# Performance work log

Hardware: AMD Instinct MI355X
Metric: run time of the kernel (lower is better)

The kernel has to match this reference:

```python
import jax, jax.numpy as jnp
import numpy as np
import math

D, NH, NL, NP_ = 256, 8, 3, 4
BS, LQ = 32, 300
SHAPES = [(80, 80), (40, 40), (20, 20)]
LV = sum(h * w for h, w in SHAPES)  # 8400
DFF = 1024


def _offset_bias():
    # faithful to MSDeformableAttention._reset_parameters
    thetas = jnp.arange(NH, dtype=jnp.float32) * (2.0 * math.pi / NH)
    grid = jnp.stack([jnp.cos(thetas), jnp.sin(thetas)], -1)
    grid = grid / jnp.abs(grid).max(-1, keepdims=True)
    grid = jnp.tile(grid.reshape(NH, 1, 1, 2), (1, NL, NP_, 1))
    grid = grid * jnp.arange(1, NP_ + 1, dtype=jnp.float32).reshape(1, 1, -1, 1)
    return grid.reshape(-1)


def setup_inputs() -> dict:
    key = jax.random.key(0)
    ks = iter(jax.random.split(key, 64))
    rn = lambda shape, s=0.02: jax.random.normal(next(ks), shape, jnp.float32) * s
    z = lambda n: jnp.zeros((n,), jnp.float32)
    o = lambda n: jnp.ones((n,), jnp.float32)
    inp = {
        'tgt': jax.random.normal(next(ks), (BS, LQ, D), jnp.float32),
        'reference_points': jax.random.uniform(next(ks), (BS, LQ, NL, 2), jnp.float32),
        'memory': jax.random.normal(next(ks), (BS, LV, D), jnp.float32),
        'query_pos_embed': jax.random.normal(next(ks), (BS, LQ, D), jnp.float32),
        'memory_spatial_shapes': np.array(SHAPES, dtype=np.int64),
        'memory_level_start_index': np.array([0, 6400, 8000], dtype=np.int64),
        # self-attn
        'Wq': rn((D, D)), 'bq': z(D), 'Wk': rn((D, D)), 'bk': z(D),
        'Wv': rn((D, D)), 'bv': z(D), 'Wo': rn((D, D)), 'bo': z(D),
        'ln1_g': o(D), 'ln1_b': z(D),
        # deformable cross-attn
        'W_vproj': rn((D, D)), 'b_vproj': z(D),
        'W_off': rn((D, NH * NL * NP_ * 2), 0.001), 'b_off': _offset_bias(),
        'W_attn': rn((D, NH * NL * NP_)), 'b_attn': z(NH * NL * NP_),
        'W_out': rn((D, D)), 'b_out': z(D),
        'ln2_g': o(D), 'ln2_b': z(D),
        # FFN
        'W1': rn((D, DFF)), 'b1': z(DFF), 'W2': rn((DFF, D)), 'b2': z(D),
        'ln3_g': o(D), 'ln3_b': z(D),
    }
    return inp


def _ln(x, g, b):
    m = x.mean(-1, keepdims=True)
    v = ((x - m) ** 2).mean(-1, keepdims=True)
    return (x - m) / jnp.sqrt(v + 1e-5) * g + b


def _ms_deform(value, shapes, loc, aw):
    # value [bs,Lv,nh,c]; loc [bs,Lq,nh,NL,NP,2] in [0,1]; aw [bs,Lq,nh,NL,NP]
    bs, Lv, nh, c = value.shape
    Lq = loc.shape[1]
    npts = loc.shape[4]
    grids = 2.0 * loc - 1.0
    out = jnp.zeros((bs, nh, Lq, c), value.dtype)
    start = 0
    for lvl, (h, w) in enumerate(shapes):
        flat = value[:, start:start + h * w].transpose(0, 2, 1, 3)  # [bs,nh,hw,c]
        start += h * w
        g = grids[:, :, :, lvl].transpose(0, 2, 1, 3, 4).reshape(bs, nh, Lq * npts, 2)
        # align_corners=False pixel coords
        x = (g[..., 0] + 1.0) * (w / 2.0) - 0.5
        y = (g[..., 1] + 1.0) * (h / 2.0) - 0.5
        x0 = jnp.floor(x); y0 = jnp.floor(y)
        wx1 = x - x0; wy1 = y - y0
        samp = jnp.zeros((bs, nh, Lq * npts, c), value.dtype)
        for xi, yi, wgt in ((x0, y0, (1 - wx1) * (1 - wy1)),
                            (x0 + 1, y0, wx1 * (1 - wy1)),
                            (x0, y0 + 1, (1 - wx1) * wy1),
                            (x0 + 1, y0 + 1, wx1 * wy1)):
            valid = (xi >= 0) & (xi < w) & (yi >= 0) & (yi < h)
            idx = (jnp.clip(yi, 0, h - 1) * w + jnp.clip(xi, 0, w - 1)).astype(jnp.int32)
            idx = jnp.broadcast_to(idx[..., None], idx.shape + (c,))
            gv = jnp.take_along_axis(flat, idx, axis=2)  # [bs,nh,Lq*np,c]
            samp = samp + gv * (wgt * valid.astype(value.dtype))[..., None]
        samp = samp.reshape(bs, nh, Lq, npts, c)
        a = aw[:, :, :, lvl].transpose(0, 2, 1, 3)  # [bs,nh,Lq,np]
        out = out + (samp * a[..., None]).sum(3)
    return out.transpose(0, 2, 1, 3).reshape(bs, Lq, nh * c)


def reference(tgt, reference_points, memory, query_pos_embed,
              memory_spatial_shapes, memory_level_start_index,
              Wq, bq, Wk, bk, Wv, bv, Wo, bo, ln1_g, ln1_b,
              W_vproj, b_vproj, W_off, b_off, W_attn, b_attn, W_out, b_out,
              ln2_g, ln2_b, W1, b1, W2, b2, ln3_g, ln3_b):
    shapes = [(int(h), int(w)) for h, w in np.asarray(memory_spatial_shapes)]
    bs, Lq, d = tgt.shape
    hd = d // NH
    # --- self attention (dropout=eval identity, attn_mask=None) ---
    q = tgt + query_pos_embed
    qh = (q @ Wq + bq).reshape(bs, Lq, NH, hd)
    kh = (q @ Wk + bk).reshape(bs, Lq, NH, hd)
    vh = (tgt @ Wv + bv).reshape(bs, Lq, NH, hd)
    att = jax.nn.softmax(jnp.einsum('bqhd,bkhd->bhqk', qh, kh) / jnp.sqrt(jnp.float32(hd)), axis=-1)
    sa = jnp.einsum('bhqk,bkhd->bqhd', att, vh).reshape(bs, Lq, d) @ Wo + bo
    tgt = _ln(tgt + sa, ln1_g, ln1_b)
    # --- deformable cross attention ---
    qc = tgt + query_pos_embed
    value = (memory @ W_vproj + b_vproj).reshape(bs, -1, NH, hd)
    off = (qc @ W_off + b_off).reshape(bs, Lq, NH, NL, NP_, 2)
    aw = jax.nn.softmax((qc @ W_attn + b_attn).reshape(bs, Lq, NH, NL * NP_), axis=-1)
    aw = aw.reshape(bs, Lq, NH, NL, NP_)
    norm = jnp.array([[w, h] for h, w in shapes], jnp.float32)  # flip -> (w,h)
    loc = reference_points[:, :, None, :, None, :] + off / norm[None, None, None, :, None, :]
    ca = _ms_deform(value, shapes, loc, aw) @ W_out + b_out
    tgt = _ln(tgt + ca, ln2_g, ln2_b)
    # --- FFN ---
    h = jax.nn.relu(tgt @ W1 + b1) @ W2 + b2
    return _ln(tgt + h, ln3_g, ln3_b)
```

## Files before the change

kernel.cpp:

```cpp
#include <hip/hip_runtime.h>
#include <hip/hip_bf16.h>

#define D_      256
#define NH_     8
#define HD_     32
#define NL_     3
#define NP_4    4
#define BS_     32
#define LQ_     300
#define LV_     8400
#define DFF_    1024
#define NTOK    (BS_ * LQ_)
#define NVAL    (BS_ * LV_)

typedef __attribute__((ext_vector_type(8))) short bf16x8;
typedef __attribute__((ext_vector_type(4))) float f32x4;

__device__ inline unsigned short f2bf(float x) {
    union { float f; unsigned u; } v; v.f = x;
    unsigned r = v.u + 0x7FFFu + ((v.u >> 16) & 1u);
    return (unsigned short)(r >> 16);
}
__device__ inline float bf2f(unsigned short x) {
    union { unsigned u; float f; } v; v.u = ((unsigned)x) << 16;
    return v.f;
}

struct TrDesc { const float* W; unsigned short* Wt; int K; int N; };
struct TrPack { TrDesc d[10]; };

__global__ __launch_bounds__(256)
void tr_kernel(TrPack p) {
    TrDesc d = p.d[blockIdx.z];
    const int n0 = blockIdx.x * 32, k0 = blockIdx.y * 32;
    if (n0 >= d.N || k0 >= d.K) return;
    __shared__ float t[32][33];
    const int tx = threadIdx.x & 31, ty = threadIdx.x >> 5;
    #pragma unroll
    for (int i = 0; i < 4; ++i) {
        int k = k0 + ty + i * 8, n = n0 + tx;
        t[ty + i * 8][tx] = (k < d.K && n < d.N) ? d.W[(size_t)k * d.N + n] : 0.f;
    }
    __syncthreads();
    #pragma unroll
    for (int i = 0; i < 4; ++i) {
        int n = n0 + ty + i * 8, k = k0 + tx;
        if (n < d.N && k < d.K) d.Wt[(size_t)n * d.K + k] = f2bf(t[tx][ty + i * 8]);
    }
}

template <int ROWS, int COLS, int KK, int KC, int WR, int WC, int AMODE, int CMODE>
__global__ __launch_bounds__(256, 4)
void gemm_os(const void* __restrict__ Ain,
             const unsigned short* __restrict__ Wt, const float* __restrict__ bias,
             void* __restrict__ Cout, int M, int N) {
    constexpr int LDK = KC + 8;
    constexpr int NC = KK / KC;
    constexpr int KS = KC / 32;
    constexpr int WROWS = ROWS / WR, WCOLS = COLS / WC;
    constexpr int RT = WROWS / 16, TC = WCOLS / 16;
    __shared__ unsigned short Alds[ROWS * LDK];
    __shared__ unsigned short Blds[COLS * LDK];

    const int tid = threadIdx.x, lane = tid & 63, w = tid >> 6;
    const int quad = lane >> 4, l16 = lane & 15;
    const int wr = w / WC, wc = w % WC;
    const int rowBase = blockIdx.y * ROWS;
    const int colBase = blockIdx.x * COLS;

    f32x4 acc[RT][TC];
    #pragma unroll
    for (int rt = 0; rt < RT; ++rt)
        #pragma unroll
        for (int j = 0; j < TC; ++j)
            #pragma unroll
            for (int r = 0; r < 4; ++r) acc[rt][j][r] = 0.f;

    for (int ch = 0; ch < NC; ++ch) {
        if (NC > 1) __syncthreads();
        if (AMODE == 2) {
            constexpr int CNT2 = ROWS * KC / 2048;
            #pragma unroll
            for (int i = 0; i < CNT2; ++i) {
                int idx = i * 256 + tid;
                int row = idx / (KC / 8), kofs = (idx % (KC / 8)) * 8;
                int4 v = *(const int4*)((const unsigned short*)Ain +
                          (size_t)(rowBase + row) * KK + ch * KC + kofs);
                *(int4*)&Alds[row * LDK + kofs] = v;
            }
        } else {
            constexpr int CNT = ROWS * KC / 1024;
            #pragma unroll
            for (int i = 0; i < CNT; ++i) {
                int idx = i * 256 + tid;
                int row = idx / (KC / 4), kofs = (idx % (KC / 4)) * 4;
                size_t gg = (size_t)(rowBase + row) * KK + ch * KC + kofs;
                float4 a = *(const float4*)((const float*)Ain + gg);
                ushort4 s4;
                s4.x = f2bf(a.x); s4.y = f2bf(a.y);
                s4.z = f2bf(a.z); s4.w = f2bf(a.w);
                *(ushort4*)&Alds[row * LDK + kofs] = s4;
            }
        }
        {
            constexpr int CNT = COLS * KC / 2048;
            #pragma unroll
            for (int i = 0; i < CNT; ++i) {
                int idx = i * 256 + tid;
                int col = idx / (KC / 8), kofs = (idx % (KC / 8)) * 8;
                int4 v = *(const int4*)(Wt + (size_t)(colBase + col) * KK + ch * KC + kofs);
                *(int4*)&Blds[col * LDK + kofs] = v;
            }
        }
        __syncthreads();

        #pragma unroll
        for (int s = 0; s < KS; ++s) {
            bf16x8 af[RT], bfr[TC];
            #pragma unroll
            for (int rt = 0; rt < RT; ++rt)
                af[rt] = *(const bf16x8*)&Alds[(wr * WROWS + rt * 16 + l16) * LDK + s * 32 + quad * 8];
            #pragma unroll
            for (int j = 0; j < TC; ++j)
                bfr[j] = *(const bf16x8*)&Blds[(wc * WCOLS + j * 16 + l16) * LDK + s * 32 + quad * 8];
            #pragma unroll
            for (int rt = 0; rt < RT; ++rt)
                #pragma unroll
                for (int j = 0; j < TC; ++j)
                    acc[rt][j] = __builtin_amdgcn_mfma_f32_16x16x32_bf16(af[rt], bfr[j], acc[rt][j], 0, 0, 0);
        }
    }

    #pragma unroll
    for (int rt = 0; rt < RT; ++rt) {
        #pragma unroll
        for (int j = 0; j < TC; ++j) {
            int col = colBase + wc * WCOLS + j * 16 + l16;
            float bb = bias[col];
            #pragma unroll
            for (int r = 0; r < 4; ++r) {
                int row = rowBase + wr * WROWS + rt * 16 + quad * 4 + r;
                float c = acc[rt][j][r] + bb;
                if (CMODE == 3) c = fmaxf(c, 0.f);
                if (CMODE >= 2)
                    ((unsigned short*)Cout)[(size_t)row * N + col] = f2bf(c);
                else
                    ((float*)Cout)[(size_t)row * N + col] = c;
            }
        }
    }
}

struct GDesc { const float* Ain; const float* A2; const unsigned short* Wt;
               const float* bias; void* Cout; int N; };
struct GPack3 { GDesc d[3]; };

template <int ROWS, int COLS, int KK, int KC, int WR, int WC, int CMODE>
__global__ __launch_bounds__(256, 4)
void gemm_osb(GPack3 pk) {
    constexpr int LDK = KC + 8;
    constexpr int NC = KK / KC;
    constexpr int KS = KC / 32;
    constexpr int WROWS = ROWS / WR, WCOLS = COLS / WC;
    constexpr int RT = WROWS / 16, TC = WCOLS / 16;
    __shared__ unsigned short Alds[ROWS * LDK];
    __shared__ unsigned short Blds[COLS * LDK];

    GDesc g = pk.d[blockIdx.z];
    const int colBase = blockIdx.x * COLS;
    if (colBase >= g.N) return;
    const int tid = threadIdx.x, lane = tid & 63, w = tid >> 6;
    const int quad = lane >> 4, l16 = lane & 15;
    const int wr = w / WC, wc = w % WC;
    const int rowBase = blockIdx.y * ROWS;

    f32x4 acc[RT][TC];
    #pragma unroll
    for (int rt = 0; rt < RT; ++rt)
        #pragma unroll
        for (int j = 0; j < TC; ++j)
            #pragma unroll
            for (int r = 0; r < 4; ++r) acc[rt][j][r] = 0.f;

    for (int ch = 0; ch < NC; ++ch) {
        if (NC > 1) __syncthreads();
        {
            constexpr int CNT = ROWS * KC / 1024;
            #pragma unroll
            for (int i = 0; i < CNT; ++i) {
                int idx = i * 256 + tid;
                int row = idx / (KC / 4), kofs = (idx % (KC / 4)) * 4;
                size_t gg = (size_t)(rowBase + row) * KK + ch * KC + kofs;
                float4 a = *(const float4*)(g.Ain + gg);
                if (g.A2) {
                    float4 b = *(const float4*)(g.A2 + gg);
                    a.x += b.x; a.y += b.y; a.z += b.z; a.w += b.w;
                }
                ushort4 s4;
                s4.x = f2bf(a.x); s4.y = f2bf(a.y);
                s4.z = f2bf(a.z); s4.w = f2bf(a.w);
                *(ushort4*)&Alds[row * LDK + kofs] = s4;
            }
        }
        {
            constexpr int CNT = COLS * KC / 2048;
            #pragma unroll
            for (int i = 0; i < CNT; ++i) {
                int idx = i * 256 + tid;
                int col = idx / (KC / 8), kofs = (idx % (KC / 8)) * 8;
                int4 v = *(const int4*)(g.Wt + (size_t)(colBase + col) * KK + ch * KC + kofs);
                *(int4*)&Blds[col * LDK + kofs] = v;
            }
        }
        __syncthreads();

        #pragma unroll
        for (int s = 0; s < KS; ++s) {
            bf16x8 af[RT], bfr[TC];
            #pragma unroll
            for (int rt = 0; rt < RT; ++rt)
                af[rt] = *(const bf16x8*)&Alds[(wr * WROWS + rt * 16 + l16) * LDK + s * 32 + quad * 8];
            #pragma unroll
            for (int j = 0; j < TC; ++j)
                bfr[j] = *(const bf16x8*)&Blds[(wc * WCOLS + j * 16 + l16) * LDK + s * 32 + quad * 8];
            #pragma unroll
            for (int rt = 0; rt < RT; ++rt)
                #pragma unroll
                for (int j = 0; j < TC; ++j)
                    acc[rt][j] = __builtin_amdgcn_mfma_f32_16x16x32_bf16(af[rt], bfr[j], acc[rt][j], 0, 0, 0);
        }
    }

    #pragma unroll
    for (int rt = 0; rt < RT; ++rt) {
        #pragma unroll
        for (int j = 0; j < TC; ++j) {
            int col = colBase + wc * WCOLS + j * 16 + l16;
            float bb = g.bias[col];
            #pragma unroll
            for (int r = 0; r < 4; ++r) {
                int row = rowBase + wr * WROWS + rt * 16 + quad * 4 + r;
                float c = acc[rt][j][r] + bb;
                if (CMODE >= 2)
                    ((unsigned short*)g.Cout)[(size_t)row * g.N + col] = f2bf(c);
                else
                    ((float*)g.Cout)[(size_t)row * g.N + col] = c;
            }
        }
    }
}

template <int KK, int KC>
__global__ __launch_bounds__(256)
void gemm_ln(const unsigned short* __restrict__ Ain,
             const unsigned short* __restrict__ Wt, const float* __restrict__ bias,
             const float* __restrict__ xres, const float* __restrict__ lng,
             const float* __restrict__ lnb, float* __restrict__ Cout) {
    constexpr int ROWS = 32, COLS = 256;
    constexpr int LDK = KC + 8;
    constexpr int NC = KK / KC;
    constexpr int KS = KC / 32;
    constexpr int RT = 2, TC = 4;
    __shared__ unsigned short Alds[ROWS * LDK];
    __shared__ unsigned short Blds[COLS * LDK];
    __shared__ float redS[4][32];
    __shared__ float redQ[4][32];

    const int tid = threadIdx.x, lane = tid & 63, w = tid >> 6;
    const int quad = lane >> 4, l16 = lane & 15;
    const int wc = w;
    const int rowBase = blockIdx.x * ROWS;

    f32x4 acc[RT][TC];
    #pragma unroll
    for (int rt = 0; rt < RT; ++rt)
        #pragma unroll
        for (int j = 0; j < TC; ++j)
            #pragma unroll
            for (int r = 0; r < 4; ++r) acc[rt][j][r] = 0.f;

    for (int ch = 0; ch < NC; ++ch) {
        if (NC > 1) __syncthreads();
        {
            constexpr int CNT2 = ROWS * KC / 2048;
            #pragma unroll
            for (int i = 0; i < CNT2; ++i) {
                int idx = i * 256 + tid;
                int row = idx / (KC / 8), kofs = (idx % (KC / 8)) * 8;
                int4 v = *(const int4*)(Ain + (size_t)(rowBase + row) * KK + ch * KC + kofs);
                *(int4*)&Alds[row * LDK + kofs] = v;
            }
        }
        {
            constexpr int CNT = COLS * KC / 2048;
            #pragma unroll
            for (int i = 0; i < CNT; ++i) {
                int idx = i * 256 + tid;
                int col = idx / (KC / 8), kofs = (idx % (KC / 8)) * 8;
                int4 v = *(const int4*)(Wt + (size_t)col * KK + ch * KC + kofs);
                *(int4*)&Blds[col * LDK + kofs] = v;
            }
        }
        __syncthreads();

        #pragma unroll
        for (int s = 0; s < KS; ++s) {
            bf16x8 af[RT], bfr[TC];
            #pragma unroll
            for (int rt = 0; rt < RT; ++rt)
                af[rt] = *(const bf16x8*)&Alds[(rt * 16 + l16) * LDK + s * 32 + quad * 8];
            #pragma unroll
            for (int j = 0; j < TC; ++j)
                bfr[j] = *(const bf16x8*)&Blds[(wc * 64 + j * 16 + l16) * LDK + s * 32 + quad * 8];
            #pragma unroll
            for (int rt = 0; rt < RT; ++rt)
                #pragma unroll
                for (int j = 0; j < TC; ++j)
                    acc[rt][j] = __builtin_amdgcn_mfma_f32_16x16x32_bf16(af[rt], bfr[j], acc[rt][j], 0, 0, 0);
        }
    }

    float p[RT][4], q[RT][4];
    #pragma unroll
    for (int rt = 0; rt < RT; ++rt)
        #pragma unroll
        for (int r = 0; r < 4; ++r) { p[rt][r] = 0.f; q[rt][r] = 0.f; }

    #pragma unroll
    for (int rt = 0; rt < RT; ++rt) {
        #pragma unroll
        for (int j = 0; j < TC; ++j) {
            int col = wc * 64 + j * 16 + l16;
            float bb = bias[col];
            #pragma unroll
            for (int r = 0; r < 4; ++r) {
                int row = rowBase + rt * 16 + quad * 4 + r;
                float v = acc[rt][j][r] + bb + xres[(size_t)row * 256 + col];
                acc[rt][j][r] = v;
                p[rt][r] += v;
                q[rt][r] += v * v;
            }
        }
    }
    #pragma unroll
    for (int rt = 0; rt < RT; ++rt)
        #pragma unroll
        for (int r = 0; r < 4; ++r)
            #pragma unroll
            for (int off = 1; off < 16; off <<= 1) {
                p[rt][r] += __shfl_xor(p[rt][r], off);
                q[rt][r] += __shfl_xor(q[rt][r], off);
            }
    if (l16 == 0) {
        #pragma unroll
        for (int rt = 0; rt < RT; ++rt)
            #pragma unroll
            for (int r = 0; r < 4; ++r) {
                redS[w][rt * 16 + quad * 4 + r] = p[rt][r];
                redQ[w][rt * 16 + quad * 4 + r] = q[rt][r];
            }
    }
    __syncthreads();
    #pragma unroll
    for (int rt = 0; rt < RT; ++rt) {
        #pragma unroll
        for (int r = 0; r < 4; ++r) {
            int ridx = rt * 16 + quad * 4 + r;
            float s  = redS[0][ridx] + redS[1][ridx] + redS[2][ridx] + redS[3][ridx];
            float ss = redQ[0][ridx] + redQ[1][ridx] + redQ[2][ridx] + redQ[3][ridx];
            float mean = s * (1.0f / 256.0f);
            float var  = ss * (1.0f / 256.0f) - mean * mean;
            float inv  = rsqrtf(var + 1e-5f);
            int row = rowBase + ridx;
            #pragma unroll
            for (int j = 0; j < TC; ++j) {
                int col = wc * 64 + j * 16 + l16;
                Cout[(size_t)row * 256 + col] =
                    (acc[rt][j][r] - mean) * inv * lng[col] + lnb[col];
            }
        }
    }
}

#define PS_STRIDE 344
__global__ __launch_bounds__(256)
void attn_mfma(const unsigned short* __restrict__ qh,
               const unsigned short* __restrict__ kh,
               const unsigned short* __restrict__ vh,
               unsigned short* __restrict__ out) {
    __shared__ unsigned short Ps[4 * 16 * PS_STRIDE];
    __shared__ unsigned short Vs[32 * PS_STRIDE];
    const int tid = threadIdx.x;
    const int bh = blockIdx.x >> 1, half_ = blockIdx.x & 1;
    const int b = bh >> 3, h = bh & 7;
    const int w = tid >> 6, lane = tid & 63;
    const int quad = lane >> 4, l16 = lane & 15;

    for (int i = tid; i < 4 * 16 * PS_STRIDE / 2; i += 256) ((unsigned*)Ps)[i] = 0u;

    const size_t hbase = ((size_t)b * LQ_) * D_ + h * HD_;
    for (int it = 0; it < 10; ++it) {
        int chunk = tid + 256 * it;
        int key = chunk >> 3, cc = (chunk & 7) * 4;
        ushort4 v = make_ushort4(0, 0, 0, 0);
        if (key < LQ_) v = *(const ushort4*)(vh + hbase + (size_t)key * D_ + cc);
        Vs[(cc + 0) * PS_STRIDE + key] = v.x;
        Vs[(cc + 1) * PS_STRIDE + key] = v.y;
        Vs[(cc + 2) * PS_STRIDE + key] = v.z;
        Vs[(cc + 3) * PS_STRIDE + key] = v.w;
    }
    __syncthreads();

    const unsigned short* qb = qh + hbase;
    const unsigned short* kb = kh + hbase;
    const float scale = 0.17677669529663687f;

    for (int qt = 10 * half_ + w; qt < 10 * half_ + 10 && qt < 19; qt += 4) {
        int rowq = qt * 16 + l16; if (rowq > LQ_ - 1) rowq = LQ_ - 1;
        bf16x8 aq = *(const bf16x8*)(qb + (size_t)rowq * D_ + quad * 8);

        f32x4 S[19];
        #pragma unroll
        for (int kt = 0; kt < 19; ++kt) {
            int rowk = kt * 16 + l16; if (rowk > LQ_ - 1) rowk = LQ_ - 1;
            bf16x8 bk = *(const bf16x8*)(kb + (size_t)rowk * D_ + quad * 8);
            f32x4 z; z[0] = z[1] = z[2] = z[3] = 0.f;
            S[kt] = __builtin_amdgcn_mfma_f32_16x16x32_bf16(aq, bk, z, 0, 0, 0);
        }
        float mrow[4] = {-1e30f, -1e30f, -1e30f, -1e30f};
        #pragma unroll
        for (int kt = 0; kt < 19; ++kt) {
            bool masked = (kt == 18) && (l16 >= 12);
            #pragma unroll
            for (int r = 0; r < 4; ++r) {
                float s = masked ? -1e30f : S[kt][r] * scale;
                S[kt][r] = s;
                mrow[r] = fmaxf(mrow[r], s);
            }
        }
        #pragma unroll
        for (int r = 0; r < 4; ++r)
            #pragma unroll
            for (int off = 1; off < 16; off <<= 1)
                mrow[r] = fmaxf(mrow[r], __shfl_xor(mrow[r], off));
        float psum[4] = {0.f, 0.f, 0.f, 0.f};
        #pragma unroll
        for (int kt = 0; kt < 19; ++kt)
            #pragma unroll
            for (int r = 0; r < 4; ++r) {
                float pcur = __expf(S[kt][r] - mrow[r]);
                S[kt][r] = pcur;
                psum[r] += pcur;
            }
        #pragma unroll
        for (int r = 0; r < 4; ++r)
            #pragma unroll
            for (int off = 1; off < 16; off <<= 1)
                psum[r] += __shfl_xor(psum[r], off);
        float linv[4];
        #pragma unroll
        for (int r = 0; r < 4; ++r) linv[r] = 1.f / psum[r];

        unsigned short* pw = Ps + w * (16 * PS_STRIDE);
        #pragma unroll
        for (int kt = 0; kt < 19; ++kt)
            #pragma unroll
            for (int r = 0; r < 4; ++r)
                pw[(quad * 4 + r) * PS_STRIDE + kt * 16 + l16] = f2bf(S[kt][r]);

        f32x4 o0, o1;
        #pragma unroll
        for (int r = 0; r < 4; ++r) { o0[r] = 0.f; o1[r] = 0.f; }
        #pragma unroll
        for (int ks = 0; ks < 10; ++ks) {
            bf16x8 ap = *(const bf16x8*)(pw + l16 * PS_STRIDE + ks * 32 + quad * 8);
            bf16x8 b0 = *(const bf16x8*)(Vs + l16 * PS_STRIDE + ks * 32 + quad * 8);
            bf16x8 b1 = *(const bf16x8*)(Vs + (16 + l16) * PS_STRIDE + ks * 32 + quad * 8);
            o0 = __builtin_amdgcn_mfma_f32_16x16x32_bf16(ap, b0, o0, 0, 0, 0);
            o1 = __builtin_amdgcn_mfma_f32_16x16x32_bf16(ap, b1, o1, 0, 0, 0);
        }
        #pragma unroll
        for (int r = 0; r < 4; ++r) {
            int q = qt * 16 + quad * 4 + r;
            if (q < LQ_) {
                size_t ob = ((size_t)b * LQ_ + q) * D_ + h * HD_;
                out[ob + l16]      = f2bf(o0[r] * linv[r]);
                out[ob + 16 + l16] = f2bf(o1[r] * linv[r]);
            }
        }
    }
}

__global__ __launch_bounds__(256)
void deform_kernel(const unsigned short* __restrict__ value,
                   const float* __restrict__ off,
                   const float* __restrict__ awl,
                   const float* __restrict__ ref,
                   unsigned short* __restrict__ out) {
    const int lvl_hw[3]    = {80, 40, 20};
    const int lvl_start[3] = {0, 6400, 8000};
    const int gid = blockIdx.x * 16 + (threadIdx.x >> 4);
    const int c2  = (threadIdx.x & 15) * 2;
    const int h   = gid & 7;
    const int bq  = gid >> 3;
    const int b   = bq / LQ_;

    float lg[12];
    const float* ap = awl + (size_t)bq * 96 + h * 12;
    float m = -1e30f;
    #pragma unroll
    for (int j = 0; j < 12; ++j) { lg[j] = ap[j]; m = fmaxf(m, lg[j]); }
    float s = 0.f;
    #pragma unroll
    for (int j = 0; j < 12; ++j) { lg[j] = __expf(lg[j] - m); s += lg[j]; }
    const float inv = 1.0f / s;

    const float* op = off + (size_t)bq * 192 + h * 24;
    const float* rp = ref + (size_t)bq * 6;

    float accx = 0.f, accy = 0.f;
    #pragma unroll
    for (int l = 0; l < NL_; ++l) {
        const int W = lvl_hw[l], H = lvl_hw[l];
        const float fw = (float)W, fh = (float)H;
        const float rx = rp[l * 2 + 0], ry = rp[l * 2 + 1];
        const unsigned short* vbase =
            value + ((size_t)b * LV_ + lvl_start[l]) * D_ + h * HD_ + c2;
        #pragma unroll
        for (int p = 0; p < NP_4; ++p) {
            float ox = op[(l * 4 + p) * 2 + 0], oy = op[(l * 4 + p) * 2 + 1];
            float x = (rx + ox / fw) * fw - 0.5f;
            float y = (ry + oy / fh) * fh - 0.5f;
            float x0f = floorf(x), y0f = floorf(y);
            float wx = x - x0f, wy = y - y0f;
            int x0 = (int)x0f, y0 = (int)y0f;
            float a = lg[l * 4 + p] * inv;
            const float cw[4] = {a * (1.f - wx) * (1.f - wy), a * wx * (1.f - wy),
                                 a * (1.f - wx) * wy,         a * wx * wy};
            const int cx[4] = {x0, x0 + 1, x0,     x0 + 1};
            const int cy[4] = {y0, y0,     y0 + 1, y0 + 1};
            #pragma unroll
            for (int cor = 0; cor < 4; ++cor) {
                int xi = cx[cor], yi = cy[cor];
                if (xi < 0 || xi >= W || yi < 0 || yi >= H) continue;
                unsigned v = *(const unsigned*)(vbase + (size_t)(yi * W + xi) * D_);
                accx += cw[cor] * bf2f((unsigned short)(v & 0xFFFFu));
                accy += cw[cor] * bf2f((unsigned short)(v >> 16));
            }
        }
    }
    unsigned pack = (unsigned)f2bf(accx) | ((unsigned)f2bf(accy) << 16);
    *(unsigned*)(out + (size_t)bq * D_ + h * HD_ + c2) = pack;
}

extern "C" void kernel_launch(void* const* d_in, const int* in_sizes, int n_in,
                              void* d_out, int out_size, void* d_ws, size_t ws_size,
                              hipStream_t stream) {
    const float* tgt   = (const float*)d_in[0];
    const float* refpt = (const float*)d_in[1];
    const float* mem   = (const float*)d_in[2];
    const float* qpos  = (const float*)d_in[3];
    const float* Wq = (const float*)d_in[6],  *bq = (const float*)d_in[7];
    const float* Wk = (const float*)d_in[8],  *bk = (const float*)d_in[9];
    const float* Wv = (const float*)d_in[10], *bv = (const float*)d_in[11];
    const float* Wo = (const float*)d_in[12], *bo = (const float*)d_in[13];
    const float* ln1_g = (const float*)d_in[14], *ln1_b = (const float*)d_in[15];
    const float* W_vproj = (const float*)d_in[16], *b_vproj = (const float*)d_in[17];
    const float* W_off  = (const float*)d_in[18], *b_off  = (const float*)d_in[19];
    const float* W_attn = (const float*)d_in[20], *b_attn = (const float*)d_in[21];
    const float* W_out  = (const float*)d_in[22], *b_out  = (const float*)d_in[23];
    const float* ln2_g = (const float*)d_in[24], *ln2_b = (const float*)d_in[25];
    const float* W1 = (const float*)d_in[26], *b1 = (const float*)d_in[27];
    const float* W2 = (const float*)d_in[28], *b2 = (const float*)d_in[29];
    const float* ln3_g = (const float*)d_in[30], *ln3_b = (const float*)d_in[31];
    float* out = (float*)d_out;

    char* p = (char*)d_ws;
    const size_t TOKD = (size_t)NTOK * D_;
    float* buf_attn = (float*)p; p += TOKD * 4;
    float* buf_tmp  = (float*)p; p += TOKD * 4;
    float* buf_t1   = (float*)p; p += TOKD * 4;
    float* buf_t2   = (float*)p; p += TOKD * 4;
    unsigned short* buf_qh = (unsigned short*)p; p += TOKD * 2;
    unsigned short* buf_kh = (unsigned short*)p; p += TOKD * 2;
    unsigned short* buf_vh = (unsigned short*)p; p += TOKD * 2;
    float* buf_off  = (float*)p; p += (size_t)NTOK * 192 * 4;
    float* buf_awl  = (float*)p; p += (size_t)NTOK * 96 * 4;
    unsigned short* wt_q   = (unsigned short*)p; p += 65536 * 2;
    unsigned short* wt_k   = (unsigned short*)p; p += 65536 * 2;
    unsigned short* wt_v   = (unsigned short*)p; p += 65536 * 2;
    unsigned short* wt_o   = (unsigned short*)p; p += 65536 * 2;
    unsigned short* wt_vp  = (unsigned short*)p; p += 65536 * 2;
    unsigned short* wt_off = (unsigned short*)p; p += 49152 * 2;
    unsigned short* wt_awl = (unsigned short*)p; p += 24576 * 2;
    unsigned short* wt_out = (unsigned short*)p; p += 65536 * 2;
    unsigned short* wt_1   = (unsigned short*)p; p += (size_t)262144 * 2;
    unsigned short* wt_2   = (unsigned short*)p; p += (size_t)262144 * 2;
    unsigned short* buf_value = (unsigned short*)p;
    unsigned short* buf_ffnb  = (unsigned short*)p;

    TrPack pk;
    pk.d[0] = {Wq,      wt_q,   256, 256};
    pk.d[1] = {Wk,      wt_k,   256, 256};
    pk.d[2] = {Wv,      wt_v,   256, 256};
    pk.d[3] = {Wo,      wt_o,   256, 256};
    pk.d[4] = {W_vproj, wt_vp,  256, 256};
    pk.d[5] = {W_off,   wt_off, 256, 192};
    pk.d[6] = {W_attn,  wt_awl, 256, 96};
    pk.d[7] = {W_out,   wt_out, 256, 256};
    pk.d[8] = {W1,      wt_1,   256, 1024};
    pk.d[9] = {W2,      wt_2,   1024, 256};
    tr_kernel<<<dim3(32, 32, 10), 256, 0, stream>>>(pk);

    GPack3 qkv;
    qkv.d[0] = {tgt, qpos,    wt_q, bq, buf_qh, 256};
    qkv.d[1] = {tgt, qpos,    wt_k, bk, buf_kh, 256};
    qkv.d[2] = {tgt, nullptr, wt_v, bv, buf_vh, 256};
    gemm_osb<32, 128, 256, 128, 1, 4, 2><<<dim3(2, NTOK / 32, 3), 256, 0, stream>>>(qkv);
    attn_mfma<<<BS_ * NH_ * 2, 256, 0, stream>>>(buf_qh, buf_kh, buf_vh,
                                                 (unsigned short*)buf_attn);
    gemm_ln<256, 128><<<NTOK / 32, 256, 0, stream>>>(
        (const unsigned short*)buf_attn, wt_o, bo, tgt, ln1_g, ln1_b, buf_t1);

    gemm_os<64, 128, 256, 128, 2, 2, 0, 2><<<dim3(2, NVAL / 64), 256, 0, stream>>>(
        mem, wt_vp, b_vproj, buf_value, NVAL, 256);
    GPack3 oa;
    oa.d[0] = {buf_t1, qpos, wt_off, b_off,  buf_off, 192};
    oa.d[1] = {buf_t1, qpos, wt_awl, b_attn, buf_awl, 96};
    oa.d[2] = oa.d[1];
    gemm_osb<32, 96, 256, 128, 2, 2, 0><<<dim3(2, NTOK / 32, 2), 256, 0, stream>>>(oa);
    deform_kernel<<<(BS_ * LQ_ * NH_) / 16, 256, 0, stream>>>(
        buf_value, buf_off, buf_awl, refpt, (unsigned short*)buf_attn);
    gemm_ln<256, 128><<<NTOK / 32, 256, 0, stream>>>(
        (const unsigned short*)buf_attn, wt_out, b_out, buf_t1, ln2_g, ln2_b, buf_t2);

    gemm_os<32, 128, 256, 128, 1, 4, 0, 3><<<dim3(8, NTOK / 32), 256, 0, stream>>>(
        buf_t2, wt_1, b1, buf_ffnb, NTOK, DFF_);
    gemm_ln<1024, 128><<<NTOK / 32, 256, 0, stream>>>(
        buf_ffnb, wt_2, b2, buf_t2, ln3_g, ln3_b, out);
}
```

Baseline: 680.6 us.

## Stream fp32 activations straight into MFMA registers, keep weights in LDS

Replaces the LDS-staged gemm_os and the QKV gemm_osb with a streaming GEMM. The full K=256 weight slice for 128 columns sits in LDS, while each wave loads its 32 rows of fp32 activations directly from global memory into registers. Those activations are converted to bf16 in registers and fed to MFMA, with a software pipeline that prefetches two K-chunks ahead. This drops A-tile LDS staging and the per-chunk barriers and uses larger 128-row blocks, in exchange for higher register pressure, a lower occupancy bound of 2, and uncoalesced strided global reads of A. NTOK=9600 divides evenly by 128, so the 128-row tiling stays valid for the token GEMMs.

```diff
diff --git a/kernel.cpp b/kernel.cpp
--- a/kernel.cpp
+++ b/kernel.cpp
@@ -49,97 +49,126 @@
     }
 }
 
-template <int ROWS, int COLS, int KK, int KC, int WR, int WC, int AMODE, int CMODE>
-__global__ __launch_bounds__(256, 4)
-void gemm_os(const void* __restrict__ Ain,
-             const unsigned short* __restrict__ Wt, const float* __restrict__ bias,
-             void* __restrict__ Cout, int M, int N) {
-    constexpr int LDK = KC + 8;
-    constexpr int NC = KK / KC;
-    constexpr int KS = KC / 32;
-    constexpr int WROWS = ROWS / WR, WCOLS = COLS / WC;
-    constexpr int RT = WROWS / 16, TC = WCOLS / 16;
-    __shared__ unsigned short Alds[ROWS * LDK];
-    __shared__ unsigned short Blds[COLS * LDK];
+template <int COLS, int AMODE, int CMODE>
+__device__ inline void gemm_stream_body(
+        const float* __restrict__ Ain, const float* __restrict__ A2,
+        const unsigned short* __restrict__ Wt, const float* __restrict__ bias,
+        void* __restrict__ Cout, int N, int colBase, int rowBase,
+        unsigned short* Blds) {
+    constexpr int LDK = 264;
+    constexpr int TC = COLS / 16;
 
     const int tid = threadIdx.x, lane = tid & 63, w = tid >> 6;
     const int quad = lane >> 4, l16 = lane & 15;
-    const int wr = w / WC, wc = w % WC;
-    const int rowBase = blockIdx.y * ROWS;
-    const int colBase = blockIdx.x * COLS;
-
-    f32x4 acc[RT][TC];
-    #pragma unroll
-    for (int rt = 0; rt < RT; ++rt)
+
+    {
+        constexpr int CNT = COLS / 8;
+        #pragma unroll
+        for (int i = 0; i < CNT; ++i) {
+            int idx = i * 256 + tid;
+            int col = idx >> 5, kofs = (idx & 31) * 8;
+            int4 v = *(const int4*)(Wt + (size_t)(colBase + col) * 256 + kofs);
+            *(int4*)&Blds[col * LDK + kofs] = v;
+        }
+    }
+    __syncthreads();
+
+    const int r0 = rowBase + w * 32 + l16;
+    const int r1 = r0 + 16;
+
+    f32x4 acc[2][TC];
+    #pragma unroll
+    for (int rt = 0; rt < 2; ++rt)
         #pragma unroll
         for (int j = 0; j < TC; ++j)
             #pragma unroll
             for (int r = 0; r < 4; ++r) acc[rt][j][r] = 0.f;
 
-    for (int ch = 0; ch < NC; ++ch) {
-        if (NC > 1) __syncthreads();
-        if (AMODE == 2) {
-            constexpr int CNT2 = ROWS * KC / 2048;
-            #pragma unroll
-            for (int i = 0; i < CNT2; ++i) {
-                int idx = i * 256 + tid;
-                int row = idx / (KC / 8), kofs = (idx % (KC / 8)) * 8;
-                int4 v = *(const int4*)((const unsigned short*)Ain +
-                          (size_t)(rowBase + row) * KK + ch * KC + kofs);
-                *(int4*)&Alds[row * LDK + kofs] = v;
-            }
-        } else {
-            constexpr int CNT = ROWS * KC / 1024;
-            #pragma unroll
-            for (int i = 0; i < CNT; ++i) {
-                int idx = i * 256 + tid;
-                int row = idx / (KC / 4), kofs = (idx % (KC / 4)) * 4;
-                size_t gg = (size_t)(rowBase + row) * KK + ch * KC + kofs;
-                float4 a = *(const float4*)((const float*)Ain + gg);
-                ushort4 s4;
-                s4.x = f2bf(a.x); s4.y = f2bf(a.y);
-                s4.z = f2bf(a.z); s4.w = f2bf(a.w);
-                *(ushort4*)&Alds[row * LDK + kofs] = s4;
-            }
-        }
-        {
-            constexpr int CNT = COLS * KC / 2048;
-            #pragma unroll
-            for (int i = 0; i < CNT; ++i) {
-                int idx = i * 256 + tid;
-                int col = idx / (KC / 8), kofs = (idx % (KC / 8)) * 8;
-                int4 v = *(const int4*)(Wt + (size_t)(colBase + col) * KK + ch * KC + kofs);
-                *(int4*)&Blds[col * LDK + kofs] = v;
-            }
-        }
-        __syncthreads();
-
-        #pragma unroll
-        for (int s = 0; s < KS; ++s) {
-            bf16x8 af[RT], bfr[TC];
-            #pragma unroll
-            for (int rt = 0; rt < RT; ++rt)
-                af[rt] = *(const bf16x8*)&Alds[(wr * WROWS + rt * 16 + l16) * LDK + s * 32 + quad * 8];
-            #pragma unroll
-            for (int j = 0; j < TC; ++j)
-                bfr[j] = *(const bf16x8*)&Blds[(wc * WCOLS + j * 16 + l16) * LDK + s * 32 + quad * 8];
-            #pragma unroll
-            for (int rt = 0; rt < RT; ++rt)
+    f32x4 rA[2][2][2], rB[2][2][2];
+    bf16x8 aA[2][2], aB[2][2];
+
+    auto loadChunk = [&](int c, f32x4 (&rr)[2][2][2]) {
+        #pragma unroll
+        for (int rt = 0; rt < 2; ++rt)
+            #pragma unroll
+            for (int s2 = 0; s2 < 2; ++s2)
                 #pragma unroll
-                for (int j = 0; j < TC; ++j)
-                    acc[rt][j] = __builtin_amdgcn_mfma_f32_16x16x32_bf16(af[rt], bfr[j], acc[rt][j], 0, 0, 0);
-        }
-    }
-
-    #pragma unroll
-    for (int rt = 0; rt < RT; ++rt) {
+                for (int hh = 0; hh < 2; ++hh) {
+                    size_t o = (size_t)(rt ? r1 : r0) * 256 +
+                               (c * 2 + s2) * 32 + quad * 8 + hh * 4;
+                    f32x4 t = *(const f32x4*)(Ain + o);
+                    if (AMODE == 1) {
+                        f32x4 u = *(const f32x4*)(A2 + o);
+                        t[0] += u[0]; t[1] += u[1]; t[2] += u[2]; t[3] += u[3];
+                    }
+                    rr[rt][s2][hh] = t;
+                }
+    };
+    auto cvtChunk = [&](const f32x4 (&rr)[2][2][2], bf16x8 (&aa)[2][2]) {
+        #pragma unroll
+        for (int rt = 0; rt < 2; ++rt)
+            #pragma unroll
+            for (int s2 = 0; s2 < 2; ++s2) {
+                bf16x8 o;
+                #pragma unroll
+                for (int e = 0; e < 4; ++e) {
+                    o[e]     = (short)f2bf(rr[rt][s2][0][e]);
+                    o[e + 4] = (short)f2bf(rr[rt][s2][1][e]);
+                }
+                aa[rt][s2] = o;
+            }
+    };
+
+    loadChunk(0, rA);
+    loadChunk(1, rB);
+    cvtChunk(rA, aA);
+    #pragma unroll
+    for (int s2 = 0; s2 < 2; ++s2)
         #pragma unroll
         for (int j = 0; j < TC; ++j) {
-            int col = colBase + wc * WCOLS + j * 16 + l16;
+            bf16x8 bfr = *(const bf16x8*)&Blds[(j * 16 + l16) * LDK + (0 * 2 + s2) * 32 + quad * 8];
+            acc[0][j] = __builtin_amdgcn_mfma_f32_16x16x32_bf16(aA[0][s2], bfr, acc[0][j], 0, 0, 0);
+            acc[1][j] = __builtin_amdgcn_mfma_f32_16x16x32_bf16(aA[1][s2], bfr, acc[1][j], 0, 0, 0);
+        }
+    loadChunk(2, rA);
+    cvtChunk(rB, aB);
+    #pragma unroll
+    for (int s2 = 0; s2 < 2; ++s2)
+        #pragma unroll
+        for (int j = 0; j < TC; ++j) {
+            bf16x8 bfr = *(const bf16x8*)&Blds[(j * 16 + l16) * LDK + (1 * 2 + s2) * 32 + quad * 8];
+            acc[0][j] = __builtin_amdgcn_mfma_f32_16x16x32_bf16(aB[0][s2], bfr, acc[0][j], 0, 0, 0);
+            acc[1][j] = __builtin_amdgcn_mfma_f32_16x16x32_bf16(aB[1][s2], bfr, acc[1][j], 0, 0, 0);
+        }
+    loadChunk(3, rB);
+    cvtChunk(rA, aA);
+    #pragma unroll
+    for (int s2 = 0; s2 < 2; ++s2)
+        #pragma unroll
+        for (int j = 0; j < TC; ++j) {
+            bf16x8 bfr = *(const bf16x8*)&Blds[(j * 16 + l16) * LDK + (2 * 2 + s2) * 32 + quad * 8];
+            acc[0][j] = __builtin_amdgcn_mfma_f32_16x16x32_bf16(aA[0][s2], bfr, acc[0][j], 0, 0, 0);
+            acc[1][j] = __builtin_amdgcn_mfma_f32_16x16x32_bf16(aA[1][s2], bfr, acc[1][j], 0, 0, 0);
+        }
+    cvtChunk(rB, aB);
+    #pragma unroll
+    for (int s2 = 0; s2 < 2; ++s2)
+        #pragma unroll
+        for (int j = 0; j < TC; ++j) {
+            bf16x8 bfr = *(const bf16x8*)&Blds[(j * 16 + l16) * LDK + (3 * 2 + s2) * 32 + quad * 8];
+            acc[0][j] = __builtin_amdgcn_mfma_f32_16x16x32_bf16(aB[0][s2], bfr, acc[0][j], 0, 0, 0);
+            acc[1][j] = __builtin_amdgcn_mfma_f32_16x16x32_bf16(aB[1][s2], bfr, acc[1][j], 0, 0, 0);
+        }
+
+    #pragma unroll
+    for (int rt = 0; rt < 2; ++rt) {
+        #pragma unroll
+        for (int j = 0; j < TC; ++j) {
+            int col = colBase + j * 16 + l16;
             float bb = bias[col];
             #pragma unroll
             for (int r = 0; r < 4; ++r) {
-                int row = rowBase + wr * WROWS + rt * 16 + quad * 4 + r;
+                int row = rowBase + w * 32 + rt * 16 + quad * 4 + r;
                 float c = acc[rt][j][r] + bb;
                 if (CMODE == 3) c = fmaxf(c, 0.f);
                 if (CMODE >= 2)
@@ -151,9 +180,32 @@
     }
 }
 
+template <int COLS, int AMODE, int CMODE>
+__global__ __launch_bounds__(256, 2)
+void gemm_stream(const float* __restrict__ Ain, const float* __restrict__ A2,
+                 const unsigned short* __restrict__ Wt, const float* __restrict__ bias,
+                 void* __restrict__ Cout, int N) {
+    __shared__ unsigned short Blds[COLS * 264];
+    gemm_stream_body<COLS, AMODE, CMODE>(Ain, A2, Wt, bias, Cout, N,
+                                         blockIdx.x * COLS, blockIdx.y * 128, Blds);
+}
+
 struct GDesc { const float* Ain; const float* A2; const unsigned short* Wt;
                const float* bias; void* Cout; int N; };
 struct GPack3 { GDesc d[3]; };
+
+template <int COLS, int CMODE>
+__global__ __launch_bounds__(256, 2)
+void gemm_streamb(GPack3 pk) {
+    __shared__ unsigned short Blds[COLS * 264];
+    GDesc g = pk.d[blockIdx.z];
+    if (g.A2)
+        gemm_stream_body<COLS, 1, CMODE>(g.Ain, g.A2, g.Wt, g.bias, g.Cout, g.N,
+                                         blockIdx.x * COLS, blockIdx.y * 128, Blds);
+    else
+        gemm_stream_body<COLS, 0, CMODE>(g.Ain, nullptr, g.Wt, g.bias, g.Cout, g.N,
+                                         blockIdx.x * COLS, blockIdx.y * 128, Blds);
+}
 
 template <int ROWS, int COLS, int KK, int KC, int WR, int WC, int CMODE>
 __global__ __launch_bounds__(256, 4)
@@ -616,14 +668,14 @@
     qkv.d[0] = {tgt, qpos,    wt_q, bq, buf_qh, 256};
     qkv.d[1] = {tgt, qpos,    wt_k, bk, buf_kh, 256};
     qkv.d[2] = {tgt, nullptr, wt_v, bv, buf_vh, 256};
-    gemm_osb<32, 128, 256, 128, 1, 4, 2><<<dim3(2, NTOK / 32, 3), 256, 0, stream>>>(qkv);
+    gemm_streamb<128, 2><<<dim3(2, NTOK / 128, 3), 256, 0, stream>>>(qkv);
     attn_mfma<<<BS_ * NH_ * 2, 256, 0, stream>>>(buf_qh, buf_kh, buf_vh,
                                                  (unsigned short*)buf_attn);
     gemm_ln<256, 128><<<NTOK / 32, 256, 0, stream>>>(
         (const unsigned short*)buf_attn, wt_o, bo, tgt, ln1_g, ln1_b, buf_t1);
 
-    gemm_os<64, 128, 256, 128, 2, 2, 0, 2><<<dim3(2, NVAL / 64), 256, 0, stream>>>(
-        mem, wt_vp, b_vproj, buf_value, NVAL, 256);
+    gemm_stream<128, 0, 2><<<dim3(2, NVAL / 128), 256, 0, stream>>>(
+        mem, nullptr, wt_vp, b_vproj, buf_value, 256);
     GPack3 oa;
     oa.d[0] = {buf_t1, qpos, wt_off, b_off,  buf_off, 192};
     oa.d[1] = {buf_t1, qpos, wt_awl, b_attn, buf_awl, 96};
@@ -634,8 +686,8 @@
     gemm_ln<256, 128><<<NTOK / 32, 256, 0, stream>>>(
         (const unsigned short*)buf_attn, wt_out, b_out, buf_t1, ln2_g, ln2_b, buf_t2);
 
-    gemm_os<32, 128, 256, 128, 1, 4, 0, 3><<<dim3(8, NTOK / 32), 256, 0, stream>>>(
-        buf_t2, wt_1, b1, buf_ffnb, NTOK, DFF_);
+    gemm_stream<128, 0, 3><<<dim3(8, NTOK / 128), 256, 0, stream>>>(
+        buf_t2, nullptr, wt_1, b1, buf_ffnb, 1024);
     gemm_ln<1024, 128><<<NTOK / 32, 256, 0, stream>>>(
         buf_ffnb, wt_2, b2, buf_t2, ln3_g, ln3_b, out);
 }
```

Result: slower. 722.2 us (+6.1%).

## Prefetch second K-chunk into registers in gemm_os and stage deform inputs in LDS

Applied to the files above, without the earlier changes.

For two-chunk fp32-input GEMMs (value projection and FFN1), the global loads for the second K chunk are issued into registers before computing the first chunk, then converted and written to LDS afterwards. This hides global load latency behind MFMA work, at the cost of more registers under a launch bound of 4 blocks per CU. The deform kernel now handles two queries per block and cooperatively loads their offsets, logits and reference points into shared memory instead of each thread reading them from global memory. A redundant leading barrier is also removed in the GEMM loops.

```diff
diff --git a/kernel.cpp b/kernel.cpp
--- a/kernel.cpp
+++ b/kernel.cpp
@@ -49,7 +49,7 @@
     }
 }
 
-template <int ROWS, int COLS, int KK, int KC, int WR, int WC, int AMODE, int CMODE>
+template <int ROWS, int COLS, int KK, int KC, int WR, int WC, int AMODE, int CMODE, int PF>
 __global__ __launch_bounds__(256, 4)
 void gemm_os(const void* __restrict__ Ain,
              const unsigned short* __restrict__ Wt, const float* __restrict__ bias,
@@ -76,8 +76,7 @@
             #pragma unroll
             for (int r = 0; r < 4; ++r) acc[rt][j][r] = 0.f;
 
-    for (int ch = 0; ch < NC; ++ch) {
-        if (NC > 1) __syncthreads();
+    auto stageA = [&](int ch) {
         if (AMODE == 2) {
             constexpr int CNT2 = ROWS * KC / 2048;
             #pragma unroll
@@ -102,18 +101,18 @@
                 *(ushort4*)&Alds[row * LDK + kofs] = s4;
             }
         }
-        {
-            constexpr int CNT = COLS * KC / 2048;
-            #pragma unroll
-            for (int i = 0; i < CNT; ++i) {
-                int idx = i * 256 + tid;
-                int col = idx / (KC / 8), kofs = (idx % (KC / 8)) * 8;
-                int4 v = *(const int4*)(Wt + (size_t)(colBase + col) * KK + ch * KC + kofs);
-                *(int4*)&Blds[col * LDK + kofs] = v;
-            }
-        }
-        __syncthreads();
-
+    };
+    auto stageB = [&](int ch) {
+        constexpr int CNT = COLS * KC / 2048;
+        #pragma unroll
+        for (int i = 0; i < CNT; ++i) {
+            int idx = i * 256 + tid;
+            int col = idx / (KC / 8), kofs = (idx % (KC / 8)) * 8;
+            int4 v = *(const int4*)(Wt + (size_t)(colBase + col) * KK + ch * KC + kofs);
+            *(int4*)&Blds[col * LDK + kofs] = v;
+        }
+    };
+    auto computeChunk = [&]() {
         #pragma unroll
         for (int s = 0; s < KS; ++s) {
             bf16x8 af[RT], bfr[TC];
@@ -128,6 +127,53 @@
                 #pragma unroll
                 for (int j = 0; j < TC; ++j)
                     acc[rt][j] = __builtin_amdgcn_mfma_f32_16x16x32_bf16(af[rt], bfr[j], acc[rt][j], 0, 0, 0);
+        }
+    };
+
+    if constexpr (PF && NC == 2 && AMODE == 0) {
+        constexpr int CNTA = ROWS * KC / 1024;
+        constexpr int CNTB = COLS * KC / 2048;
+        stageA(0); stageB(0);
+        __syncthreads();
+        float4 pa[CNTA]; int4 pb[CNTB];
+        #pragma unroll
+        for (int i = 0; i < CNTA; ++i) {
+            int idx = i * 256 + tid;
+            int row = idx / (KC / 4), kofs = (idx % (KC / 4)) * 4;
+            pa[i] = *(const float4*)((const float*)Ain +
+                     (size_t)(rowBase + row) * KK + KC + kofs);
+        }
+        #pragma unroll
+        for (int i = 0; i < CNTB; ++i) {
+            int idx = i * 256 + tid;
+            int col = idx / (KC / 8), kofs = (idx % (KC / 8)) * 8;
+            pb[i] = *(const int4*)(Wt + (size_t)(colBase + col) * KK + KC + kofs);
+        }
+        computeChunk();
+        __syncthreads();
+        #pragma unroll
+        for (int i = 0; i < CNTA; ++i) {
+            int idx = i * 256 + tid;
+            int row = idx / (KC / 4), kofs = (idx % (KC / 4)) * 4;
+            ushort4 s4;
+            s4.x = f2bf(pa[i].x); s4.y = f2bf(pa[i].y);
+            s4.z = f2bf(pa[i].z); s4.w = f2bf(pa[i].w);
+            *(ushort4*)&Alds[row * LDK + kofs] = s4;
+        }
+        #pragma unroll
+        for (int i = 0; i < CNTB; ++i) {
+            int idx = i * 256 + tid;
+            int col = idx / (KC / 8), kofs = (idx % (KC / 8)) * 8;
+            *(int4*)&Blds[col * LDK + kofs] = pb[i];
+        }
+        __syncthreads();
+        computeChunk();
+    } else {
+        for (int ch = 0; ch < NC; ++ch) {
+            if (NC > 1 && ch > 0) __syncthreads();
+            stageA(ch); stageB(ch);
+            __syncthreads();
+            computeChunk();
         }
     }
 
@@ -183,7 +229,7 @@
             for (int r = 0; r < 4; ++r) acc[rt][j][r] = 0.f;
 
     for (int ch = 0; ch < NC; ++ch) {
-        if (NC > 1) __syncthreads();
+        if (NC > 1 && ch > 0) __syncthreads();
         {
             constexpr int CNT = ROWS * KC / 1024;
             #pragma unroll
@@ -280,7 +326,7 @@
             for (int r = 0; r < 4; ++r) acc[rt][j][r] = 0.f;
 
     for (int ch = 0; ch < NC; ++ch) {
-        if (NC > 1) __syncthreads();
+        if (NC > 1 && ch > 0) __syncthreads();
         {
             constexpr int CNT2 = ROWS * KC / 2048;
             #pragma unroll
@@ -499,24 +545,38 @@
                    unsigned short* __restrict__ out) {
     const int lvl_hw[3]    = {80, 40, 20};
     const int lvl_start[3] = {0, 6400, 8000};
-    const int gid = blockIdx.x * 16 + (threadIdx.x >> 4);
-    const int c2  = (threadIdx.x & 15) * 2;
-    const int h   = gid & 7;
-    const int bq  = gid >> 3;
+    __shared__ float offL[2][192];
+    __shared__ float awlL[2][96];
+    __shared__ float refL[2][6];
+
+    const int tid = threadIdx.x;
+    const int bq0 = blockIdx.x * 2;
+    if (tid < 96)
+        ((float4*)&offL[0][0])[tid] = ((const float4*)(off + (size_t)bq0 * 192))[tid];
+    else if (tid < 144)
+        ((float4*)&awlL[0][0])[tid - 96] = ((const float4*)(awl + (size_t)bq0 * 96))[tid - 96];
+    else if (tid < 156)
+        (&refL[0][0])[tid - 144] = (ref + (size_t)bq0 * 6)[tid - 144];
+    __syncthreads();
+
+    const int g16 = tid >> 4;
+    const int c2  = (tid & 15) * 2;
+    const int lb  = g16 >> 3;
+    const int h   = g16 & 7;
+    const int bq  = bq0 + lb;
     const int b   = bq / LQ_;
 
     float lg[12];
-    const float* ap = awl + (size_t)bq * 96 + h * 12;
     float m = -1e30f;
     #pragma unroll
-    for (int j = 0; j < 12; ++j) { lg[j] = ap[j]; m = fmaxf(m, lg[j]); }
+    for (int j = 0; j < 12; ++j) { lg[j] = awlL[lb][h * 12 + j]; m = fmaxf(m, lg[j]); }
     float s = 0.f;
     #pragma unroll
     for (int j = 0; j < 12; ++j) { lg[j] = __expf(lg[j] - m); s += lg[j]; }
     const float inv = 1.0f / s;
 
-    const float* op = off + (size_t)bq * 192 + h * 24;
-    const float* rp = ref + (size_t)bq * 6;
+    const float* op = &offL[lb][h * 24];
+    const float* rp = &refL[lb][0];
 
     float accx = 0.f, accy = 0.f;
     #pragma unroll
@@ -622,19 +682,19 @@
     gemm_ln<256, 128><<<NTOK / 32, 256, 0, stream>>>(
         (const unsigned short*)buf_attn, wt_o, bo, tgt, ln1_g, ln1_b, buf_t1);
 
-    gemm_os<64, 128, 256, 128, 2, 2, 0, 2><<<dim3(2, NVAL / 64), 256, 0, stream>>>(
+    gemm_os<64, 128, 256, 128, 2, 2, 0, 2, 1><<<dim3(2, NVAL / 64), 256, 0, stream>>>(
         mem, wt_vp, b_vproj, buf_value, NVAL, 256);
     GPack3 oa;
     oa.d[0] = {buf_t1, qpos, wt_off, b_off,  buf_off, 192};
     oa.d[1] = {buf_t1, qpos, wt_awl, b_attn, buf_awl, 96};
     oa.d[2] = oa.d[1];
     gemm_osb<32, 96, 256, 128, 2, 2, 0><<<dim3(2, NTOK / 32, 2), 256, 0, stream>>>(oa);
-    deform_kernel<<<(BS_ * LQ_ * NH_) / 16, 256, 0, stream>>>(
+    deform_kernel<<<NTOK / 2, 256, 0, stream>>>(
         buf_value, buf_off, buf_awl, refpt, (unsigned short*)buf_attn);
     gemm_ln<256, 128><<<NTOK / 32, 256, 0, stream>>>(
         (const unsigned short*)buf_attn, wt_out, b_out, buf_t1, ln2_g, ln2_b, buf_t2);
 
-    gemm_os<32, 128, 256, 128, 1, 4, 0, 3><<<dim3(8, NTOK / 32), 256, 0, stream>>>(
+    gemm_os<32, 128, 256, 128, 1, 4, 0, 3, 1><<<dim3(8, NTOK / 32), 256, 0, stream>>>(
         buf_t2, wt_1, b1, buf_ffnb, NTOK, DFF_);
     gemm_ln<1024, 128><<<NTOK / 32, 256, 0, stream>>>(
         buf_ffnb, wt_2, b2, buf_t2, ln3_g, ln3_b, out);
```

New measurement: 787.7 us. 1.16x slower.
